# Kernel optimization log

Hardware: AMD Instinct MI355X
Metric: run time of the kernel (lower is better)

The kernel has to match this reference:

```python
import jax, jax.numpy as jnp
import numpy as np

NUM_HEADS = 8
CH_PER_HEAD = 32
NUM_GROUPS = 32
EPS = 1e-5
SCALE = CH_PER_HEAD ** (-0.25)


def group_norm(x, scale, bias):
    # x: [b, c, h, w]
    b, c, h, w = x.shape
    xg = x.reshape(b, NUM_GROUPS, c // NUM_GROUPS, h, w)
    mean = xg.mean(axis=(2, 3, 4), keepdims=True)
    var = xg.var(axis=(2, 3, 4), keepdims=True)
    xg = (xg - mean) * jax.lax.rsqrt(var + EPS)
    x = xg.reshape(b, c, h, w)
    return x * scale[None, :, None, None] + bias[None, :, None, None]


def conv1x1(x, w, b):
    # x: [b, c_in, n], w: [c_out, c_in], b: [c_out]
    return jnp.einsum('oc,bcn->bon', w, x) + b[None, :, None]


def setup_inputs() -> dict:
    key = jax.random.key(0)
    ks = jax.random.split(key, 12)
    c_in, c_out, hid = 256, 256, NUM_HEADS * CH_PER_HEAD
    d = {}
    d['x'] = jax.random.normal(ks[0], (2, c_in, 64, 64), dtype=jnp.float32)
    d['gn_scale'] = jnp.ones((c_in,), dtype=jnp.float32)
    d['gn_bias'] = jnp.zeros((c_in,), dtype=jnp.float32)
    def lin(k, co, ci):
        return jax.random.normal(k, (co, ci), dtype=jnp.float32) * (ci ** -0.5)
    d['wq'] = lin(ks[1], hid, c_in)
    d['bq'] = jnp.zeros((hid,), dtype=jnp.float32)
    d['wk'] = lin(ks[2], hid, c_in)
    d['bk'] = jnp.zeros((hid,), dtype=jnp.float32)
    d['wv'] = lin(ks[3], hid, c_in)
    d['bv'] = jnp.zeros((hid,), dtype=jnp.float32)
    # Original zero-inits to_out; we use small random weights so the
    # attention path contributes to the output (non-trivial baseline).
    d['wo'] = lin(ks[4], c_out, hid) * 0.02
    d['bo'] = jnp.zeros((c_out,), dtype=jnp.float32)
    return d


def reference(x, gn_scale, gn_bias, wq, bq, wk, bk, wv, bv, wo, bo):
    b, c, h, w = x.shape
    n = h * w
    x_n = group_norm(x, gn_scale, gn_bias).reshape(b, c, n)
    q = conv1x1(x_n, wq, bq)  # [b, hid, n]
    k = conv1x1(x_n, wk, bk)
    v = conv1x1(x_n, wv, bv)
    def split_heads(t):
        return t.reshape(b, NUM_HEADS, CH_PER_HEAD, n)
    q, k, v = split_heads(q) * SCALE, split_heads(k) * SCALE, split_heads(v)
    attn = jax.nn.softmax(jnp.einsum('bhdi,bhdj->bhij', q, k), axis=-1)
    out = jnp.einsum('bhij,bhdj->bhdi', attn, v)  # [b, h, d, n]
    out = out.reshape(b, NUM_HEADS * CH_PER_HEAD, n)
    out = conv1x1(out, wo, bo).reshape(b, -1, h, w)
    return x + out
```

## Files before the change

kernel.cpp:

```cpp
#include <hip/hip_runtime.h>

#define C 256
#define N 4096
#define CPG 8
#define GE (CPG * N)
#define JL 2048

constexpr float EPS = 1e-5f;
constexpr float QK_SCALE_E = 0.50500979f;

typedef float f32x4 __attribute__((ext_vector_type(4)));
typedef short s16x8 __attribute__((ext_vector_type(8)));

__device__ __forceinline__ short f2bf(float f) {
    union { float f; unsigned u; } v; v.f = f;
    unsigned r = v.u + 0x7FFFu + ((v.u >> 16) & 1u);
    return (short)(r >> 16);
}
__device__ __forceinline__ float bf2f(short s) {
    union { unsigned u; float f; } v; v.u = ((unsigned)(unsigned short)s) << 16;
    return v.f;
}

__global__ __launch_bounds__(1024) void k_stats(const float* __restrict__ x,
                                                float2* __restrict__ stats) {
    int b = blockIdx.x >> 5, g = blockIdx.x & 31;
    size_t base = (size_t)(b * C + g * CPG) * N;
    const float* xp = x + base;
    int tid = threadIdx.x;
    float sum = 0.f, ss = 0.f;
    for (int i = tid * 4; i < GE; i += 4096) {
        float4 v = *(const float4*)(xp + i);
        sum += (v.x + v.y) + (v.z + v.w);
        ss  += (v.x * v.x + v.y * v.y) + (v.z * v.z + v.w * v.w);
    }
    #pragma unroll
    for (int o = 32; o; o >>= 1) {
        sum += __shfl_down(sum, o, 64);
        ss  += __shfl_down(ss, o, 64);
    }
    __shared__ float red[32];
    int wid = tid >> 6;
    if ((tid & 63) == 0) { red[wid] = sum; red[16 + wid] = ss; }
    __syncthreads();
    if (tid == 0) {
        sum = 0.f; ss = 0.f;
        #pragma unroll
        for (int i = 0; i < 16; ++i) { sum += red[i]; ss += red[16 + i]; }
        float mean = sum * (1.f / GE);
        float var  = ss * (1.f / GE) - mean * mean;
        stats[b * 32 + g] = make_float2(mean, rsqrtf(var + EPS));
    }
}

__global__ __launch_bounds__(256) void k_wcvt(const float* __restrict__ wq,
        const float* __restrict__ wk, const float* __restrict__ wv,
        const float* __restrict__ wo, short* __restrict__ wqkvb,
        short* __restrict__ wob) {
    int i = blockIdx.x * 256 + threadIdx.x;
    if (i < 65536)       wqkvb[i] = f2bf(wq[i]);
    else if (i < 131072) wqkvb[i] = f2bf(wk[i - 65536]);
    else if (i < 196608) wqkvb[i] = f2bf(wv[i - 131072]);
    else                 wob[i - 196608] = f2bf(wo[i - 196608]);
}

__global__ __launch_bounds__(256) void k_t(const float* __restrict__ x,
        const float* __restrict__ gs, const float* __restrict__ gb,
        const float2* __restrict__ stats, short* __restrict__ xnT) {
    __shared__ __align__(16) short lt[64][72];
    int id = blockIdx.x;
    int b  = id >> 8;
    int ct = (id >> 6) & 3;
    int nt = id & 63;
    int c0 = ct * 64, n0 = nt * 64;
    int t = threadIdx.x;
    int cc = t >> 2;
    int c = c0 + cc;
    float2 st = stats[b * 32 + (c >> 3)];
    float sc = gs[c] * st.y;
    float bi = gb[c] - st.x * sc;
    const float* xp = x + (size_t)(b * C + c) * N + n0;
    #pragma unroll
    for (int it = 0; it < 4; ++it) {
        int f4 = (t & 3) + it * 4;
        float4 v = *(const float4*)(xp + f4 * 4);
        int nl = f4 * 4;
        lt[nl + 0][cc] = f2bf(v.x * sc + bi);
        lt[nl + 1][cc] = f2bf(v.y * sc + bi);
        lt[nl + 2][cc] = f2bf(v.z * sc + bi);
        lt[nl + 3][cc] = f2bf(v.w * sc + bi);
    }
    __syncthreads();
    int nl = t >> 2, seg = t & 3;
    short* op = xnT + (size_t)(b * N + n0 + nl) * C + c0 + seg * 16;
    s16x8 w0 = *(const s16x8*)&lt[nl][seg * 16];
    s16x8 w1 = *(const s16x8*)&lt[nl][seg * 16 + 8];
    *(s16x8*)op = w0;
    *(s16x8*)(op + 8) = w1;
}

__global__ __launch_bounds__(256) void k_qkv(const short* __restrict__ wqkvb,
        const short* __restrict__ xnT, const float* __restrict__ bq,
        const float* __restrict__ bk, const float* __restrict__ bv,
        short* __restrict__ qT, short* __restrict__ kT, short* __restrict__ vB) {
    __shared__ __align__(16) short bs[64 * 256];
    __shared__ __align__(16) short lt[4][64][16];
    int nb = blockIdx.x, mb = blockIdx.y, b = blockIdx.z;
    int m0 = mb * 64, n0 = nb * 64;
    int t = threadIdx.x;
    int wid = t >> 6, lane = t & 63;
    int lr = lane & 15, lg = lane >> 4;
    int mw = m0 + wid * 16;

    const short* ap_ = wqkvb + (mw + lr) * C + lg * 8;
    s16x8 af[8];
    #pragma unroll
    for (int kk = 0; kk < 8; ++kk)
        af[kk] = *(const s16x8*)(ap_ + kk * 32);

    {
        int gr = t >> 2;
        const short* gp = xnT + ((size_t)b * N + n0 + gr) * C + (t & 3) * 8;
        #pragma unroll
        for (int i = 0; i < 8; ++i) {
            int sl = (t & 3) + 4 * i;
            s16x8 v = *(const s16x8*)(gp + 32 * i);
            *(s16x8*)&bs[gr * 256 + ((sl ^ (gr & 7)) * 8)] = v;
        }
    }
    __syncthreads();

    f32x4 acc[4] = {{0,0,0,0},{0,0,0,0},{0,0,0,0},{0,0,0,0}};
    #pragma unroll
    for (int kk = 0; kk < 8; ++kk) {
        int sb = kk * 4;
        #pragma unroll
        for (int f = 0; f < 4; ++f) {
            int row = f * 16 + lr;
            s16x8 xf = *(const s16x8*)&bs[row * 256 + (((sb + lg) ^ (lr & 7)) * 8)];
            acc[f] = __builtin_amdgcn_mfma_f32_16x16x32_bf16(af[kk], xf, acc[f], 0, 0, 0);
        }
    }

    int kind = mb >> 2;
    const float* bias = kind == 0 ? bq : (kind == 1 ? bk : bv);
    int mloc = mw - kind * 256;
    float bvals[4];
    #pragma unroll
    for (int r = 0; r < 4; ++r) bvals[r] = bias[mloc + 4 * lg + r];
    int h = mloc >> 5;
    if (kind == 2) {
        short* vbase = vB + (size_t)((b * 8 + h) * 32) * N;
        #pragma unroll
        for (int f = 0; f < 4; ++f) {
            int n = n0 + f * 16 + lr;
            #pragma unroll
            for (int r = 0; r < 4; ++r) {
                int dd = (mloc & 31) + 4 * lg + r;
                vbase[(size_t)dd * N + n] = f2bf(acc[f][r] + bvals[r]);
            }
        }
    } else {
        short* dst = (kind == 0) ? qT : kT;
        #pragma unroll
        for (int f = 0; f < 4; ++f)
            #pragma unroll
            for (int r = 0; r < 4; ++r)
                lt[wid][f * 16 + lr][4 * lg + r] =
                    f2bf((acc[f][r] + bvals[r]) * QK_SCALE_E);
        int ln = lane;
        s16x8 w0 = *(const s16x8*)&lt[wid][ln][0];
        s16x8 w1 = *(const s16x8*)&lt[wid][ln][8];
        short* op = dst + ((size_t)(b * 8 + h) * N + n0 + ln) * 32 + (mloc & 16);
        *(s16x8*)op = w0;
        *(s16x8*)(op + 8) = w1;
    }
}

#define EXPB(d, s_) asm("v_exp_f32 %0, %1\n\ts_nop 0" : "=v"(d) : "v"(s_))

#define TILE_BODY() do {                                                          \
    f32x4 s0 = __builtin_amdgcn_mfma_f32_16x16x32_bf16(bk0, aq, zero, 0, 0, 0);   \
    f32x4 s1 = __builtin_amdgcn_mfma_f32_16x16x32_bf16(bk1, aq, zero, 0, 0, 0);   \
    float e00, e01, e02, e03, e10, e11, e12, e13;                                 \
    EXPB(e00, s0[0]); EXPB(e01, s0[1]); EXPB(e02, s0[2]); EXPB(e03, s0[3]);       \
    EXPB(e10, s1[0]); EXPB(e11, s1[1]); EXPB(e12, s1[2]); EXPB(e13, s1[3]);       \
    unsigned w0, w1, w2, w3;                                                      \
    asm("v_cvt_pk_bf16_f32 %0, %1, %2" : "=v"(w0) : "v"(e00), "v"(e01));          \
    asm("v_cvt_pk_bf16_f32 %0, %1, %2" : "=v"(w1) : "v"(e02), "v"(e03));          \
    asm("v_cvt_pk_bf16_f32 %0, %1, %2" : "=v"(w2) : "v"(e10), "v"(e11));          \
    asm("v_cvt_pk_bf16_f32 %0, %1, %2" : "=v"(w3) : "v"(e12), "v"(e13));          \
    asm("v_permlane32_swap_b32 %0, %1" : "+v"(w0), "+v"(w2));                     \
    asm("v_permlane16_swap_b32 %0, %1" : "+v"(w0), "+v"(w2));                     \
    asm("v_permlane32_swap_b32 %0, %1" : "+v"(w1), "+v"(w3));                     \
    asm("v_permlane16_swap_b32 %0, %1" : "+v"(w1), "+v"(w3));                     \
    union { int4 i4; s16x8 s8; } apu;                                             \
    apu.i4 = make_int4((int)w0, (int)w1, (int)w2, (int)w3);                       \
    s16x8 ap = apu.s8;                                                            \
    lac = __builtin_amdgcn_mfma_f32_16x16x32_bf16(ap, ones, lac, 0, 0, 0);        \
    o0  = __builtin_amdgcn_mfma_f32_16x16x32_bf16(ap, bv0, o0, 0, 0, 0);          \
    o1  = __builtin_amdgcn_mfma_f32_16x16x32_bf16(ap, bv1, o1, 0, 0, 0);          \
} while (0)

__global__ __launch_bounds__(256, 8) void k_attn(const short* __restrict__ qT,
        const short* __restrict__ kT, const short* __restrict__ vB,
        short* __restrict__ po0, short* __restrict__ po1,
        float* __restrict__ pl) {
    __shared__ __align__(16) short pool[8192];
    int xb  = blockIdx.x;
    int rm  = (xb & 7) * 128 + (xb >> 3);
    int bh  = rm >> 6;
    int wid = threadIdx.x >> 6;
    int i0  = (rm & 63) * 64 + wid * 16;
    int s   = blockIdx.y;
    int jb  = s * JL;
    int lane = threadIdx.x & 63;
    int lr = lane & 15, lg = lane >> 4;
    const short* qTb = qT + (size_t)bh * N * 32;
    const short* kTb = kT + (size_t)bh * N * 32;
    const short* vBb = vB + (size_t)bh * 32 * N;

    s16x8 aq = *(const s16x8*)(qTb + (i0 + lr) * 32 + lg * 8);
    s16x8 ones;
    #pragma unroll
    for (int e = 0; e < 8; ++e) ones[e] = (short)0x3F80;

    f32x4 o0 = {0,0,0,0}, o1 = {0,0,0,0}, lac = {0,0,0,0};
    const f32x4 zero = {0,0,0,0};

    int krow  = 16 * wid + (lane >> 2);
    int kslot = lane & 3;
    const short* kg = kTb + (size_t)(jb + krow) * 32 + kslot * 8;
    int kw_ofs = krow * 32 + ((kslot ^ (krow & 3)) * 8);

    int vrow  = 8 * wid + (lane >> 3);
    int vslot = lane & 7;
    const short* vg = vBb + (size_t)vrow * N + jb + vslot * 8;
    int vw_ofs = vrow * 64 + ((vslot ^ (vrow & 7)) * 8);

    int kr_base = lr * 32 + ((lg ^ (lr & 3)) * 8);
    int vr0 = lr * 64, vr1 = (16 + lr) * 64;
    int sw0 = ((0 + lg) ^ (lr & 7)) * 8;
    int sw1 = ((4 + lg) ^ (lr & 7)) * 8;

    {
        s16x8 kreg = *(const s16x8*)kg;
        s16x8 vreg = *(const s16x8*)vg;
        *(s16x8*)&pool[kw_ofs] = kreg;
        *(s16x8*)&pool[4096 + vw_ofs] = vreg;
    }
    __syncthreads();

    for (int t = 0; t < 32; ++t) {
        int p = t & 1;
        s16x8 nk, nv;
        if (t < 31) {
            nk = *(const s16x8*)(kg + (t + 1) * 2048);
            nv = *(const s16x8*)(vg + (t + 1) * 64);
        }
        const short* lkp = &pool[p * 2048];
        const short* lvp = &pool[4096 + p * 2048];
        {
            s16x8 bk0 = *(const s16x8*)(lkp + kr_base);
            s16x8 bk1 = *(const s16x8*)(lkp + 512 + kr_base);
            s16x8 bv0 = *(const s16x8*)(lvp + vr0 + sw0);
            s16x8 bv1 = *(const s16x8*)(lvp + vr1 + sw0);
            TILE_BODY();
        }
        {
            s16x8 bk0 = *(const s16x8*)(lkp + 1024 + kr_base);
            s16x8 bk1 = *(const s16x8*)(lkp + 1536 + kr_base);
            s16x8 bv0 = *(const s16x8*)(lvp + vr0 + sw1);
            s16x8 bv1 = *(const s16x8*)(lvp + vr1 + sw1);
            TILE_BODY();
        }
        if (t < 31) {
            int q = (t + 1) & 1;
            *(s16x8*)&pool[q * 2048 + kw_ofs] = nk;
            *(s16x8*)&pool[4096 + q * 2048 + vw_ofs] = nv;
        }
        __syncthreads();
    }

    #pragma unroll
    for (int r = 0; r < 4; ++r) {
        pool[wid * 640 + (4 * lg + r) * 40 + lr]      = f2bf(o0[r]);
        pool[wid * 640 + (4 * lg + r) * 40 + 16 + lr] = f2bf(o1[r]);
    }
    if (lr == 0) {
        float* plp = pl + ((size_t)(s * 16 + bh)) * N + i0;
        #pragma unroll
        for (int r = 0; r < 4; ++r) plp[4 * lg + r] = lac[r];
    }
    short* pob = s ? po1 : po0;
    int il = lane >> 2, seg = lane & 3;
    s16x8 w = *(const s16x8*)&pool[wid * 640 + il * 40 + seg * 8];
    short* op = pob + ((size_t)bh * N + i0 + il) * 32 + seg * 8;
    *(s16x8*)op = w;
}

__global__ __launch_bounds__(256) void k_out(const short* __restrict__ wob,
        const short* __restrict__ po0, const short* __restrict__ po1,
        const float* __restrict__ pl, const float* __restrict__ bo,
        const float* __restrict__ x, float* __restrict__ out) {
    __shared__ __align__(16) short bs[8 * 64 * 32];
    int nb = blockIdx.x, mb = blockIdx.y, b = blockIdx.z;
    int n0 = nb * 64;
    int t = threadIdx.x;
    int wid = t >> 6, lane = t & 63;
    int lr = lane & 15, lg = lane >> 4;
    int mw = mb * 64 + wid * 16;

    const short* ap_ = wob + (mw + lr) * C + lg * 8;
    s16x8 af[8];
    #pragma unroll
    for (int h = 0; h < 8; ++h) af[h] = *(const s16x8*)(ap_ + h * 32);

    {
        int h = t >> 5, idx = t & 31;
        size_t rb = ((size_t)(b * 8 + h)) * N + n0;
        const short* g0 = po0 + rb * 32;
        const short* g1 = po1 + rb * 32;
        const float* pl0 = pl + rb;
        const float* pl1 = pl + (size_t)16 * N * 16 / 16 * 1;
        pl1 = pl + ((size_t)(16 + b * 8 + h)) * N + n0;
        #pragma unroll
        for (int i = 0; i < 8; ++i) {
            int chunk = idx + 32 * i;
            int r = chunk >> 2, sl = chunk & 3;
            s16x8 v0 = *(const s16x8*)(g0 + r * 32 + sl * 8);
            s16x8 v1 = *(const s16x8*)(g1 + r * 32 + sl * 8);
            float inv = 1.f / (pl0[r] + pl1[r]);
            s16x8 w;
            #pragma unroll
            for (int e = 0; e < 8; ++e)
                w[e] = f2bf((bf2f(v0[e]) + bf2f(v1[e])) * inv);
            *(s16x8*)&bs[h * 2048 + r * 32 + ((sl ^ (r & 3)) * 8)] = w;
        }
    }
    __syncthreads();

    f32x4 acc[4] = {{0,0,0,0},{0,0,0,0},{0,0,0,0},{0,0,0,0}};
    #pragma unroll
    for (int h = 0; h < 8; ++h) {
        #pragma unroll
        for (int f = 0; f < 4; ++f) {
            int row = f * 16 + lr;
            s16x8 xf = *(const s16x8*)&bs[h * 2048 + row * 32 + ((lg ^ (lr & 3)) * 8)];
            acc[f] = __builtin_amdgcn_mfma_f32_16x16x32_bf16(af[h], xf, acc[f], 0, 0, 0);
        }
    }

    float bvals[4];
    #pragma unroll
    for (int r = 0; r < 4; ++r) bvals[r] = bo[mw + 4 * lg + r];
    #pragma unroll
    for (int f = 0; f < 4; ++f) {
        int n = n0 + f * 16 + lr;
        #pragma unroll
        for (int r = 0; r < 4; ++r) {
            size_t idx = (size_t)(b * C + mw + 4 * lg + r) * N + n;
            out[idx] = acc[f][r] + bvals[r] + x[idx];
        }
    }
}

extern "C" void kernel_launch(void* const* d_in, const int* in_sizes, int n_in,
                              void* d_out, int out_size, void* d_ws, size_t ws_size,
                              hipStream_t stream) {
    const float* x  = (const float*)d_in[0];
    const float* gs = (const float*)d_in[1];
    const float* gb = (const float*)d_in[2];
    const float* wq = (const float*)d_in[3];
    const float* bq = (const float*)d_in[4];
    const float* wk = (const float*)d_in[5];
    const float* bk = (const float*)d_in[6];
    const float* wv = (const float*)d_in[7];
    const float* bv = (const float*)d_in[8];
    const float* wo = (const float*)d_in[9];
    const float* bo = (const float*)d_in[10];
    float* out = (float*)d_out;
    char* ws = (char*)d_ws;

    float2* stats = (float2*)(ws);
    short*  wqkvb = (short*)(ws + 0x1000);
    float*  pl    = (float*)(ws + 0x1000);
    short*  wob   = (short*)(ws + 0x81000);
    short*  xnT   = (short*)(ws + 0xB0000);
    short*  po1   = (short*)(ws + 0xB0000);
    short*  qT    = (short*)(ws + 0x4B0000);
    short*  kT    = (short*)(ws + 0x8B0000);
    short*  vB    = (short*)(ws + 0xCB0000);
    short*  po0   = (short*)(ws + 0x10B0000);

    k_stats<<<64, 1024, 0, stream>>>(x, stats);
    k_wcvt <<<1024, 256, 0, stream>>>(wq, wk, wv, wo, wqkvb, wob);
    k_t    <<<512, 256, 0, stream>>>(x, gs, gb, stats, xnT);
    k_qkv  <<<dim3(64, 12, 2), 256, 0, stream>>>(wqkvb, xnT, bq, bk, bv, qT, kT, vB);
    k_attn <<<dim3(1024, 2), 256, 0, stream>>>(qT, kT, vB, po0, po1, pl);
    k_out  <<<dim3(64, 4, 2), 256, 0, stream>>>(wob, po0, po1, pl, bo, x, out);
}
```

Baseline: 165.2 us.

## Split groupnorm stats, stage V stores via LDS, retile k_out and reorder grids

```diff
diff --git a/kernel.cpp b/kernel.cpp
--- a/kernel.cpp
+++ b/kernel.cpp
@@ -22,14 +22,14 @@
     return v.f;
 }
 
-__global__ __launch_bounds__(1024) void k_stats(const float* __restrict__ x,
-                                                float2* __restrict__ stats) {
-    int b = blockIdx.x >> 5, g = blockIdx.x & 31;
-    size_t base = (size_t)(b * C + g * CPG) * N;
+__global__ __launch_bounds__(256) void k_stats(const float* __restrict__ x,
+                                               float2* __restrict__ partials) {
+    int q = blockIdx.x & 3, g = (blockIdx.x >> 2) & 31, b = blockIdx.x >> 7;
+    size_t base = (size_t)(b * C + g * CPG) * N + q * (GE / 4);
     const float* xp = x + base;
     int tid = threadIdx.x;
     float sum = 0.f, ss = 0.f;
-    for (int i = tid * 4; i < GE; i += 4096) {
+    for (int i = tid * 4; i < GE / 4; i += 1024) {
         float4 v = *(const float4*)(xp + i);
         sum += (v.x + v.y) + (v.z + v.w);
         ss  += (v.x * v.x + v.y * v.y) + (v.z * v.z + v.w * v.w);
@@ -39,17 +39,14 @@
         sum += __shfl_down(sum, o, 64);
         ss  += __shfl_down(ss, o, 64);
     }
-    __shared__ float red[32];
+    __shared__ float red[8];
     int wid = tid >> 6;
-    if ((tid & 63) == 0) { red[wid] = sum; red[16 + wid] = ss; }
+    if ((tid & 63) == 0) { red[wid] = sum; red[4 + wid] = ss; }
     __syncthreads();
     if (tid == 0) {
-        sum = 0.f; ss = 0.f;
-        #pragma unroll
-        for (int i = 0; i < 16; ++i) { sum += red[i]; ss += red[16 + i]; }
-        float mean = sum * (1.f / GE);
-        float var  = ss * (1.f / GE) - mean * mean;
-        stats[b * 32 + g] = make_float2(mean, rsqrtf(var + EPS));
+        sum = red[0] + red[1] + red[2] + red[3];
+        ss  = red[4] + red[5] + red[6] + red[7];
+        partials[(b * 32 + g) * 4 + q] = make_float2(sum, ss);
     }
 }
 
@@ -66,7 +63,7 @@
 
 __global__ __launch_bounds__(256) void k_t(const float* __restrict__ x,
         const float* __restrict__ gs, const float* __restrict__ gb,
-        const float2* __restrict__ stats, short* __restrict__ xnT) {
+        const float2* __restrict__ partials, short* __restrict__ xnT) {
     __shared__ __align__(16) short lt[64][72];
     int id = blockIdx.x;
     int b  = id >> 8;
@@ -76,9 +73,16 @@
     int t = threadIdx.x;
     int cc = t >> 2;
     int c = c0 + cc;
-    float2 st = stats[b * 32 + (c >> 3)];
-    float sc = gs[c] * st.y;
-    float bi = gb[c] - st.x * sc;
+    int bg = b * 32 + (c >> 3);
+    float2 p0 = partials[bg * 4 + 0], p1 = partials[bg * 4 + 1];
+    float2 p2 = partials[bg * 4 + 2], p3 = partials[bg * 4 + 3];
+    float sum = (p0.x + p1.x) + (p2.x + p3.x);
+    float ss  = (p0.y + p1.y) + (p2.y + p3.y);
+    float mean = sum * (1.f / GE);
+    float var  = ss * (1.f / GE) - mean * mean;
+    float rstd = rsqrtf(var + EPS);
+    float sc = gs[c] * rstd;
+    float bi = gb[c] - mean * sc;
     const float* xp = x + (size_t)(b * C + c) * N + n0;
     #pragma unroll
     for (int it = 0; it < 4; ++it) {
@@ -105,7 +109,7 @@
         short* __restrict__ qT, short* __restrict__ kT, short* __restrict__ vB) {
     __shared__ __align__(16) short bs[64 * 256];
     __shared__ __align__(16) short lt[4][64][16];
-    int nb = blockIdx.x, mb = blockIdx.y, b = blockIdx.z;
+    int mb = blockIdx.x, nb = blockIdx.y, b = blockIdx.z;
     int m0 = mb * 64, n0 = nb * 64;
     int t = threadIdx.x;
     int wid = t >> 6, lane = t & 63;
@@ -150,16 +154,26 @@
     for (int r = 0; r < 4; ++r) bvals[r] = bias[mloc + 4 * lg + r];
     int h = mloc >> 5;
     if (kind == 2) {
-        short* vbase = vB + (size_t)((b * 8 + h) * 32) * N;
-        #pragma unroll
-        for (int f = 0; f < 4; ++f) {
-            int n = n0 + f * 16 + lr;
+        short (*vt)[64] = (short(*)[64])lt;
+        #pragma unroll
+        for (int f = 0; f < 4; ++f)
             #pragma unroll
             for (int r = 0; r < 4; ++r) {
-                int dd = (mloc & 31) + 4 * lg + r;
-                vbase[(size_t)dd * N + n] = f2bf(acc[f][r] + bvals[r]);
+                int rl = wid * 16 + 4 * lg + r;
+                int cn = f * 16 + lr;
+                int sl = cn >> 3, off = cn & 7;
+                vt[rl][((sl ^ (rl & 7)) * 8) + off] = f2bf(acc[f][r] + bvals[r]);
             }
-        }
+        __syncthreads();
+        int mlocB = mb * 64 - 512;
+        int h0 = mlocB >> 5;
+        int rr = t >> 2, sl = t & 3;
+        int h2 = h0 + (rr >> 5), dd = rr & 31;
+        short* vdst = vB + ((size_t)((b * 8 + h2) * 32 + dd)) * N + n0;
+        s16x8 w0v = *(const s16x8*)&vt[rr][(sl ^ (rr & 7)) * 8];
+        s16x8 w1v = *(const s16x8*)&vt[rr][((sl + 4) ^ (rr & 7)) * 8];
+        *(s16x8*)(vdst + sl * 8) = w0v;
+        *(s16x8*)(vdst + (sl + 4) * 8) = w1v;
     } else {
         short* dst = (kind == 0) ? qT : kT;
         #pragma unroll
@@ -303,9 +317,9 @@
         const short* __restrict__ po0, const short* __restrict__ po1,
         const float* __restrict__ pl, const float* __restrict__ bo,
         const float* __restrict__ x, float* __restrict__ out) {
-    __shared__ __align__(16) short bs[8 * 64 * 32];
-    int nb = blockIdx.x, mb = blockIdx.y, b = blockIdx.z;
-    int n0 = nb * 64;
+    __shared__ __align__(16) short bs[8 * 32 * 32];
+    int mb = blockIdx.x, nb = blockIdx.y, b = blockIdx.z;
+    int n0 = nb * 32;
     int t = threadIdx.x;
     int wid = t >> 6, lane = t & 63;
     int lr = lane & 15, lg = lane >> 4;
@@ -322,10 +336,9 @@
         const short* g0 = po0 + rb * 32;
         const short* g1 = po1 + rb * 32;
         const float* pl0 = pl + rb;
-        const float* pl1 = pl + (size_t)16 * N * 16 / 16 * 1;
-        pl1 = pl + ((size_t)(16 + b * 8 + h)) * N + n0;
-        #pragma unroll
-        for (int i = 0; i < 8; ++i) {
+        const float* pl1 = pl + ((size_t)(16 + b * 8 + h)) * N + n0;
+        #pragma unroll
+        for (int i = 0; i < 4; ++i) {
             int chunk = idx + 32 * i;
             int r = chunk >> 2, sl = chunk & 3;
             s16x8 v0 = *(const s16x8*)(g0 + r * 32 + sl * 8);
@@ -335,18 +348,18 @@
             #pragma unroll
             for (int e = 0; e < 8; ++e)
                 w[e] = f2bf((bf2f(v0[e]) + bf2f(v1[e])) * inv);
-            *(s16x8*)&bs[h * 2048 + r * 32 + ((sl ^ (r & 3)) * 8)] = w;
+            *(s16x8*)&bs[h * 1024 + r * 32 + ((sl ^ (r & 3)) * 8)] = w;
         }
     }
     __syncthreads();
 
-    f32x4 acc[4] = {{0,0,0,0},{0,0,0,0},{0,0,0,0},{0,0,0,0}};
+    f32x4 acc[2] = {{0,0,0,0},{0,0,0,0}};
     #pragma unroll
     for (int h = 0; h < 8; ++h) {
         #pragma unroll
-        for (int f = 0; f < 4; ++f) {
+        for (int f = 0; f < 2; ++f) {
             int row = f * 16 + lr;
-            s16x8 xf = *(const s16x8*)&bs[h * 2048 + row * 32 + ((lg ^ (lr & 3)) * 8)];
+            s16x8 xf = *(const s16x8*)&bs[h * 1024 + row * 32 + ((lg ^ (lr & 3)) * 8)];
             acc[f] = __builtin_amdgcn_mfma_f32_16x16x32_bf16(af[h], xf, acc[f], 0, 0, 0);
         }
     }
@@ -355,7 +368,7 @@
     #pragma unroll
     for (int r = 0; r < 4; ++r) bvals[r] = bo[mw + 4 * lg + r];
     #pragma unroll
-    for (int f = 0; f < 4; ++f) {
+    for (int f = 0; f < 2; ++f) {
         int n = n0 + f * 16 + lr;
         #pragma unroll
         for (int r = 0; r < 4; ++r) {
@@ -382,7 +395,7 @@
     float* out = (float*)d_out;
     char* ws = (char*)d_ws;
 
-    float2* stats = (float2*)(ws);
+    float2* partials = (float2*)(ws);
     short*  wqkvb = (short*)(ws + 0x1000);
     float*  pl    = (float*)(ws + 0x1000);
     short*  wob   = (short*)(ws + 0x81000);
@@ -393,10 +406,10 @@
     short*  vB    = (short*)(ws + 0xCB0000);
     short*  po0   = (short*)(ws + 0x10B0000);
 
-    k_stats<<<64, 1024, 0, stream>>>(x, stats);
+    k_stats<<<256, 256, 0, stream>>>(x, partials);
     k_wcvt <<<1024, 256, 0, stream>>>(wq, wk, wv, wo, wqkvb, wob);
-    k_t    <<<512, 256, 0, stream>>>(x, gs, gb, stats, xnT);
-    k_qkv  <<<dim3(64, 12, 2), 256, 0, stream>>>(wqkvb, xnT, bq, bk, bv, qT, kT, vB);
+    k_t    <<<512, 256, 0, stream>>>(x, gs, gb, partials, xnT);
+    k_qkv  <<<dim3(12, 64, 2), 256, 0, stream>>>(wqkvb, xnT, bq, bk, bv, qT, kT, vB);
     k_attn <<<dim3(1024, 2), 256, 0, stream>>>(qT, kT, vB, po0, po1, pl);
-    k_out  <<<dim3(64, 4, 2), 256, 0, stream>>>(wob, po0, po1, pl, bo, x, out);
-}
+    k_out  <<<dim3(4, 128, 2), 256, 0, stream>>>(wob, po0, po1, pl, bo, x, out);
+}
```

Result: faster. 158.8 us (-3.9%).
